# Performance work log

Hardware: AMD Instinct MI355X
Metric: run time of the kernel (lower is better)

The kernel has to match this reference:

```python
import jax, jax.numpy as jnp
import numpy as np

# --- constants (structural / non-tensor args of run()) ---
B = 1024        # number of independent systems (replicas)
NDOF = 64       # degrees of freedom per system (x0.shape[-1])
N_CHAIN = 2     # thermostat chain length
DT = 0.002      # integration time step
N_STEPS = 200   # number of MD steps


def force_fn(x):
    # harmonic potential U = 0.5*|x|^2  ->  F = -x
    return -x


def setup_inputs() -> dict:
    key = jax.random.key(0)
    k1, k2 = jax.random.split(key)
    x0 = jax.random.normal(k1, (B, NDOF), dtype=jnp.float32)
    v0 = jax.random.normal(k2, (B, NDOF), dtype=jnp.float32)
    kT = jnp.ones((), dtype=jnp.float32)
    mass = jnp.ones((), dtype=jnp.float32)
    Q = jnp.ones((), dtype=jnp.float32)
    return {"x0": x0, "v0": v0, "kT": kT, "mass": mass, "Q": Q}


def _nhc_step(x, v, xi, kT, mass, Q):
    dt = DT
    ndof = NDOF
    # xi: (..., N_CHAIN)
    KE = 0.5 * mass * jnp.sum(v * v, axis=-1)            # (...,)
    G = (2.0 * KE - ndof * kT) / Q
    xi_list = [xi[..., j] for j in range(N_CHAIN)]
    # first half chain update, j = n_chain-1 .. 0 (staggered half steps)
    for j in range(N_CHAIN - 1, -1, -1):
        if j == N_CHAIN - 1:
            xi_list[j] = xi_list[j] + dt / 4 * G
        else:
            s = jnp.exp(-xi_list[j + 1] * dt / 8)
            xi_list[j] = (xi_list[j] * s + dt / 4 * G) * s
        if j == 0:
            v = v * jnp.exp(-xi_list[0][..., None] * dt / 2)
            KE = 0.5 * mass * jnp.sum(v * v, axis=-1)
        G = (2.0 * KE - ndof * kT) / Q if j == 0 else (Q * xi_list[j - 1] ** 2 - kT) / Q
    # velocity-Verlet inner step
    v = v + dt / 2 * force_fn(x) / mass
    x = x + dt * v
    v = v + dt / 2 * force_fn(x) / mass
    KE = 0.5 * mass * jnp.sum(v * v, axis=-1)
    G = (2.0 * KE - ndof * kT) / Q
    # second half chain update, j = 0 .. n_chain-1
    for j in range(N_CHAIN):
        if j == 0:
            v = v * jnp.exp(-xi_list[0][..., None] * dt / 2)
            KE = 0.5 * mass * jnp.sum(v * v, axis=-1)
            G = (2.0 * KE - ndof * kT) / Q
        if j == N_CHAIN - 1:
            xi_list[j] = xi_list[j] + dt / 4 * G
        else:
            s = jnp.exp(-xi_list[j + 1] * dt / 8)
            xi_list[j] = (xi_list[j] * s + dt / 4 * G) * s
        G = (Q * xi_list[j] ** 2 - kT) / Q
    return x, v, jnp.stack(xi_list, axis=-1)


def _run(x0, v0, kT, mass, Q):
    xi0 = jnp.zeros(x0.shape[:-1] + (N_CHAIN,), dtype=x0.dtype)

    def body(carry, _):
        x, v, xi = carry
        x, v, xi = _nhc_step(x, v, xi, kT, mass, Q)
        return (x, v, xi), (x, v)

    _, (xs, vs) = jax.lax.scan(body, (x0, v0, xi0), xs=None, length=N_STEPS)
    traj_x = jnp.concatenate([x0[None], xs], axis=0)   # (N_STEPS+1, B, NDOF)
    traj_v = jnp.concatenate([v0[None], vs], axis=0)
    return traj_x, traj_v


def reference(x0, v0, kT, mass, Q):
    return _run(x0, v0, kT, mass, Q)
```

## Files before the change

kernel.cpp:

```cpp
#include <hip/hip_runtime.h>

#define NB     1024
#define NDOF   64
#define NSTEPS 200
#define DTF    0.002f

__global__ __launch_bounds__(256) void nhc_kernel(
    const float* __restrict__ x0, const float* __restrict__ v0,
    const float* __restrict__ kTp, const float* __restrict__ massp,
    const float* __restrict__ Qp, float* __restrict__ out)
{
    const int tid  = blockIdx.x * blockDim.x + threadIdx.x;
    const int sys  = tid >> 6;
    const int lane = tid & 63;
    if (sys >= NB) return;

    const float kT   = kTp[0];
    const float mass = massp[0];
    const float Q    = Qp[0];

    const float dt     = DTF;
    const float dt2    = 0.5f   * DTF;
    const float dt4    = 0.25f  * DTF;
    const float dt8    = 0.125f * DTF;
    const float invQ   = 1.0f / Q;
    const float c      = dt2 / mass;
    const float c2     = c * c;
    const float dtdt   = dt * dt;
    const float ndofkT = (float)NDOF * kT;
    const float kTQ    = kT * invQ;

    float x = x0[sys * NDOF + lane];
    float v = v0[sys * NDOF + lane];
    float xi0 = 0.0f, xi1 = 0.0f;

    float* __restrict__ out_x = out;
    float* __restrict__ out_v = out + (size_t)(NSTEPS + 1) * NB * NDOF;

    out_x[sys * NDOF + lane] = x;
    out_v[sys * NDOF + lane] = v;

    float Sxx = x * x, Sxv = x * v, Svv = v * v;
    #pragma unroll
    for (int off = 32; off; off >>= 1) {
        Sxx += __shfl_xor(Sxx, off, 64);
        Sxv += __shfl_xor(Sxv, off, 64);
        Svv += __shfl_xor(Svv, off, 64);
    }

    float Gk = (mass * Svv - ndofkT) * invQ;

    size_t widx = (size_t)NB * NDOF + sys * NDOF + lane;

    for (int n = 0; n < NSTEPS; ++n) {
        xi1 = fmaf(dt4, Gk, xi1);
        float s  = __expf(-xi1 * dt8);
        float G0 = fmaf(Q * xi0, xi0, -kT) * invQ;
        xi0 = fmaf(xi0, s, dt4 * G0) * s;
        float sc = __expf(-xi0 * dt2);
        float sc2 = sc * sc;

        v *= sc;
        v = fmaf(-c, x, v);
        x = fmaf(dt, v, x);
        v = fmaf(-c, x, v);
        v *= sc;

        Svv *= sc2;  Sxv *= sc;
        float Svv1 = fmaf(c2, Sxx, fmaf(-2.0f * c, Sxv, Svv));
        float Sxv1 = fmaf(-c, Sxx, Sxv);
        float Sxx1 = fmaf(dtdt, Svv1, fmaf(2.0f * dt, Sxv1, Sxx));
        float Sxv2 = fmaf(dt, Svv1, Sxv1);
        float Svv2 = fmaf(c2, Sxx1, fmaf(-2.0f * c, Sxv2, Svv1));
        float Sxv3 = fmaf(-c, Sxx1, Sxv2);
        Svv = Svv2 * sc2;  Sxv = Sxv3 * sc;  Sxx = Sxx1;

        float Gt = (mass * Svv - ndofkT) * invQ;
        xi0 = fmaf(xi0, s, dt4 * Gt) * s;
        float G1 = fmaf(Q * xi0, xi0, -kT) * invQ;
        xi1 = fmaf(dt4, G1, xi1);
        Gk = Gt;

        out_x[widx] = x;
        out_v[widx] = v;
        widx += (size_t)NB * NDOF;
    }
    (void)kTQ;
}

extern "C" void kernel_launch(void* const* d_in, const int* in_sizes, int n_in,
                              void* d_out, int out_size, void* d_ws, size_t ws_size,
                              hipStream_t stream) {
    const float* x0   = (const float*)d_in[0];
    const float* v0   = (const float*)d_in[1];
    const float* kT   = (const float*)d_in[2];
    const float* mass = (const float*)d_in[3];
    const float* Q    = (const float*)d_in[4];
    float* out = (float*)d_out;

    const int total = NB * NDOF;
    const int block = 256;
    const int grid  = total / block;
    nhc_kernel<<<grid, block, 0, stream>>>(x0, v0, kT, mass, Q, out);
}
```

Baseline: 123.7 us.

## Split NHC integration into per-system propagator scan and parallel trajectory expansion

The per-step linear update of (x, v) becomes a 2x2 propagator matrix that is accumulated per system in a first kernel, using only the scalar moment recurrence. A second, fully parallel kernel applies each step's matrix to the initial x0 and v0 and writes the whole trajectory with float4 stores across all steps. The goal is to stop the output write of about 100 MB from being bound to a sequential 200-step loop with low parallelism and scalar stores. It needs a workspace, falls back to the fused kernel when the workspace is too small, and may drift numerically from the step-by-step recurrence.

Result: slower. 140.6 us (+13.7%).

```diff
diff --git a/kernel.cpp b/kernel.cpp
--- a/kernel.cpp
+++ b/kernel.cpp
@@ -5,10 +5,10 @@
 #define NSTEPS 200
 #define DTF    0.002f
 
-__global__ __launch_bounds__(256) void nhc_kernel(
+__global__ __launch_bounds__(256) void nhc_phase1(
     const float* __restrict__ x0, const float* __restrict__ v0,
     const float* __restrict__ kTp, const float* __restrict__ massp,
-    const float* __restrict__ Qp, float* __restrict__ out)
+    const float* __restrict__ Qp, float4* __restrict__ P)
 {
     const int tid  = blockIdx.x * blockDim.x + threadIdx.x;
     const int sys  = tid >> 6;
@@ -28,17 +28,12 @@
     const float c2     = c * c;
     const float dtdt   = dt * dt;
     const float ndofkT = (float)NDOF * kT;
-    const float kTQ    = kT * invQ;
-
-    float x = x0[sys * NDOF + lane];
-    float v = v0[sys * NDOF + lane];
+    const float alpha  = 1.0f - dt * c;
+    const float gamma  = -c * (2.0f - dt * c);
+
+    const float x = x0[sys * NDOF + lane];
+    const float v = v0[sys * NDOF + lane];
     float xi0 = 0.0f, xi1 = 0.0f;
-
-    float* __restrict__ out_x = out;
-    float* __restrict__ out_v = out + (size_t)(NSTEPS + 1) * NB * NDOF;
-
-    out_x[sys * NDOF + lane] = x;
-    out_v[sys * NDOF + lane] = v;
 
     float Sxx = x * x, Sxv = x * v, Svv = v * v;
     #pragma unroll
@@ -50,21 +45,15 @@
 
     float Gk = (mass * Svv - ndofkT) * invQ;
 
-    size_t widx = (size_t)NB * NDOF + sys * NDOF + lane;
+    float p00 = 1.0f, p01 = 0.0f, p10 = 0.0f, p11 = 1.0f;
 
     for (int n = 0; n < NSTEPS; ++n) {
         xi1 = fmaf(dt4, Gk, xi1);
         float s  = __expf(-xi1 * dt8);
         float G0 = fmaf(Q * xi0, xi0, -kT) * invQ;
         xi0 = fmaf(xi0, s, dt4 * G0) * s;
-        float sc = __expf(-xi0 * dt2);
+        float sc  = __expf(-xi0 * dt2);
         float sc2 = sc * sc;
-
-        v *= sc;
-        v = fmaf(-c, x, v);
-        x = fmaf(dt, v, x);
-        v = fmaf(-c, x, v);
-        v *= sc;
 
         Svv *= sc2;  Sxv *= sc;
         float Svv1 = fmaf(c2, Sxx, fmaf(-2.0f * c, Sxv, Svv));
@@ -81,11 +70,112 @@
         xi1 = fmaf(dt4, G1, xi1);
         Gk = Gt;
 
-        out_x[widx] = x;
-        out_v[widx] = v;
-        widx += (size_t)NB * NDOF;
-    }
-    (void)kTQ;
+        float b  = dt * sc;
+        float g  = gamma * sc;
+        float a2 = alpha * sc2;
+        float q00 = fmaf(alpha, p00, b * p10);
+        float q01 = fmaf(alpha, p01, b * p11);
+        float q10 = fmaf(g,     p00, a2 * p10);
+        float q11 = fmaf(g,     p01, a2 * p11);
+        p00 = q00; p01 = q01; p10 = q10; p11 = q11;
+
+        if (lane == 0) P[sys * NSTEPS + n] = make_float4(p00, p01, p10, p11);
+    }
+}
+
+#define F4_PER_SYS (NDOF / 4)
+#define F4_PER_STEP (NB * F4_PER_SYS)
+#define TOTAL_F4 ((NSTEPS + 1) * F4_PER_STEP)
+
+__global__ __launch_bounds__(256) void nhc_phase2(
+    const float* __restrict__ x0, const float* __restrict__ v0,
+    const float4* __restrict__ P, float* __restrict__ out)
+{
+    const int t = blockIdx.x * blockDim.x + threadIdx.x;
+    if (t >= TOTAL_F4) return;
+
+    const int step = t / F4_PER_STEP;
+    const int rem  = t - step * F4_PER_STEP;
+    const int sys  = rem >> 4;
+    const int q    = rem & 15;
+
+    const float4 xv = *reinterpret_cast<const float4*>(&x0[sys * NDOF + q * 4]);
+    const float4 vv = *reinterpret_cast<const float4*>(&v0[sys * NDOF + q * 4]);
+
+    const size_t o = (size_t)step * (NB * NDOF) + sys * NDOF + q * 4;
+    float4* __restrict__ ox = reinterpret_cast<float4*>(&out[o]);
+    float4* __restrict__ ov = reinterpret_cast<float4*>(
+        &out[o + (size_t)(NSTEPS + 1) * NB * NDOF]);
+
+    if (step == 0) {
+        *ox = xv;
+        *ov = vv;
+        return;
+    }
+    const float4 p = P[sys * NSTEPS + (step - 1)];
+    float4 rx, rv;
+    rx.x = fmaf(p.x, xv.x, p.y * vv.x);  rv.x = fmaf(p.z, xv.x, p.w * vv.x);
+    rx.y = fmaf(p.x, xv.y, p.y * vv.y);  rv.y = fmaf(p.z, xv.y, p.w * vv.y);
+    rx.z = fmaf(p.x, xv.z, p.y * vv.z);  rv.z = fmaf(p.z, xv.z, p.w * vv.z);
+    rx.w = fmaf(p.x, xv.w, p.y * vv.w);  rv.w = fmaf(p.z, xv.w, p.w * vv.w);
+    *ox = rx;
+    *ov = rv;
+}
+
+__global__ __launch_bounds__(256) void nhc_fused(
+    const float* __restrict__ x0, const float* __restrict__ v0,
+    const float* __restrict__ kTp, const float* __restrict__ massp,
+    const float* __restrict__ Qp, float* __restrict__ out)
+{
+    const int tid  = blockIdx.x * blockDim.x + threadIdx.x;
+    const int sys  = tid >> 6;
+    const int lane = tid & 63;
+    if (sys >= NB) return;
+
+    const float kT = kTp[0], mass = massp[0], Q = Qp[0];
+    const float dt = DTF, dt2 = 0.5f*DTF, dt4 = 0.25f*DTF, dt8 = 0.125f*DTF;
+    const float invQ = 1.0f/Q, c = dt2/mass, c2 = c*c, dtdt = dt*dt;
+    const float ndofkT = (float)NDOF * kT;
+
+    float x = x0[sys*NDOF+lane], v = v0[sys*NDOF+lane];
+    float xi0 = 0.0f, xi1 = 0.0f;
+    float* __restrict__ out_x = out;
+    float* __restrict__ out_v = out + (size_t)(NSTEPS+1)*NB*NDOF;
+    out_x[sys*NDOF+lane] = x;  out_v[sys*NDOF+lane] = v;
+
+    float Sxx = x*x, Sxv = x*v, Svv = v*v;
+    #pragma unroll
+    for (int off = 32; off; off >>= 1) {
+        Sxx += __shfl_xor(Sxx, off, 64);
+        Sxv += __shfl_xor(Sxv, off, 64);
+        Svv += __shfl_xor(Svv, off, 64);
+    }
+    float Gk = (mass*Svv - ndofkT) * invQ;
+    size_t widx = (size_t)NB*NDOF + sys*NDOF + lane;
+
+    for (int n = 0; n < NSTEPS; ++n) {
+        xi1 = fmaf(dt4, Gk, xi1);
+        float s  = __expf(-xi1*dt8);
+        float G0 = fmaf(Q*xi0, xi0, -kT) * invQ;
+        xi0 = fmaf(xi0, s, dt4*G0) * s;
+        float sc = __expf(-xi0*dt2), sc2 = sc*sc;
+        v *= sc;  v = fmaf(-c,x,v);  x = fmaf(dt,v,x);  v = fmaf(-c,x,v);  v *= sc;
+        Svv *= sc2;  Sxv *= sc;
+        float Svv1 = fmaf(c2,Sxx,fmaf(-2.0f*c,Sxv,Svv));
+        float Sxv1 = fmaf(-c,Sxx,Sxv);
+        float Sxx1 = fmaf(dtdt,Svv1,fmaf(2.0f*dt,Sxv1,Sxx));
+        float Sxv2 = fmaf(dt,Svv1,Sxv1);
+        float Svv2 = fmaf(c2,Sxx1,fmaf(-2.0f*c,Sxv2,Svv1));
+        float Sxv3 = fmaf(-c,Sxx1,Sxv2);
+        Svv = Svv2*sc2;  Sxv = Sxv3*sc;  Sxx = Sxx1;
+        float Gt = (mass*Svv - ndofkT) * invQ;
+        xi0 = fmaf(xi0, s, dt4*Gt) * s;
+        float G1 = fmaf(Q*xi0, xi0, -kT) * invQ;
+        xi1 = fmaf(dt4, G1, xi1);
+        Gk = Gt;
+        out_x[widx] = x;  out_v[widx] = v;
+        widx += (size_t)NB*NDOF;
+    }
 }
 
 extern "C" void kernel_launch(void* const* d_in, const int* in_sizes, int n_in,
@@ -98,8 +188,15 @@
     const float* Q    = (const float*)d_in[4];
     float* out = (float*)d_out;
 
-    const int total = NB * NDOF;
-    const int block = 256;
-    const int grid  = total / block;
-    nhc_kernel<<<grid, block, 0, stream>>>(x0, v0, kT, mass, Q, out);
-}
+    const size_t ws_needed = (size_t)NB * NSTEPS * 4 * sizeof(float);
+    if (ws_size < ws_needed) {
+        nhc_fused<<<NB * NDOF / 256, 256, 0, stream>>>(x0, v0, kT, mass, Q, out);
+        return;
+    }
+    float4* P = (float4*)d_ws;
+
+    nhc_phase1<<<NB * NDOF / 256, 256, 0, stream>>>(x0, v0, kT, mass, Q, P);
+
+    const int blocks = (TOTAL_F4 + 255) / 256;
+    nhc_phase2<<<blocks, 256, 0, stream>>>(x0, v0, P, out);
+}
```
